# Kernel tuning notes

Hardware: AMD Instinct MI355X
Metric: run time of the kernel (lower is better)

The kernel has to match this reference:

```python
import jax, jax.numpy as jnp
import numpy as np

B, A, NB, BOND = 256, 100, 10, 110
AF, BF, H, DEPTH = 82, 6, 300, 3

def setup_inputs() -> dict:
    key = jax.random.key(0)
    ks = jax.random.split(key, 16)
    atom_feats = jax.random.normal(ks[0], (B, A, AF), dtype=jnp.float32)
    bond_feats = jax.random.normal(ks[1], (B, BOND, BF), dtype=jnp.float32)
    ag_b = jax.random.randint(ks[2], (B, A, NB, 1), 0, B, dtype=jnp.int32)
    ag_a = jax.random.randint(ks[3], (B, A, NB, 1), 0, A, dtype=jnp.int32)
    atom_graph = jnp.concatenate([ag_b, ag_a], axis=-1)
    bg_b = jax.random.randint(ks[4], (B, A, NB, 1), 0, B, dtype=jnp.int32)
    bg_e = jax.random.randint(ks[5], (B, A, NB, 1), 0, BOND, dtype=jnp.int32)
    bond_graph = jnp.concatenate([bg_b, bg_e], axis=-1)
    num_nbs = jax.random.randint(ks[6], (B, A), 0, NB + 1, dtype=jnp.int32)
    n_atoms = jax.random.randint(ks[7], (B,), 50, A + 1, dtype=jnp.int32)
    n_atoms = n_atoms.at[0].set(A)  # padding must equal n_atoms.max()
    sc = lambda i, o: (2.0 / (i + o)) ** 0.5
    w_fc1 = jax.random.normal(ks[8], (AF, H), dtype=jnp.float32) * sc(AF, H)
    w_nei = jax.random.normal(ks[9], (H + BF, H), dtype=jnp.float32) * sc(H + BF, H)
    b_nei = jnp.zeros((H,), dtype=jnp.float32)
    w_atom = jax.random.normal(ks[10], (2 * H, H), dtype=jnp.float32) * sc(2 * H, H)
    b_atom = jnp.zeros((H,), dtype=jnp.float32)
    w2a = jax.random.normal(ks[11], (H, H), dtype=jnp.float32) * sc(H, H)
    w2b = jax.random.normal(ks[12], (BF, H), dtype=jnp.float32) * sc(BF, H)
    w_fc2 = jax.random.normal(ks[13], (H, H), dtype=jnp.float32) * sc(H, H)
    return dict(atom_feats=atom_feats, bond_feats=bond_feats, w_fc1=w_fc1,
                w_nei=w_nei, b_nei=b_nei, w_atom=w_atom, b_atom=b_atom,
                w2a=w2a, w2b=w2b, w_fc2=w_fc2, atom_graph=atom_graph,
                bond_graph=bond_graph, num_nbs=num_nbs, n_atoms=n_atoms)

def reference(atom_feats, bond_feats, w_fc1, w_nei, b_nei, w_atom, b_atom,
              w2a, w2b, w_fc2, atom_graph, bond_graph, num_nbs, n_atoms):
    h = jax.nn.relu(atom_feats @ w_fc1)                      # [B,A,H]
    bondnei = bond_feats[bond_graph[..., 0], bond_graph[..., 1]]  # [B,A,NB,BF]
    mask_neis = (num_nbs[..., None] > jnp.arange(NB, dtype=jnp.int32))[..., None]
    mask_atoms = (n_atoms[:, None] > jnp.arange(A, dtype=jnp.int32))[..., None]
    for i in range(DEPTH):
        atomnei = h[atom_graph[..., 0], atom_graph[..., 1]]  # [B,A,NB,H]
        if i + 1 == DEPTH:
            nei = (atomnei @ w2a) * (bondnei @ w2b)          # [B,A,NB,H]
            nei = jnp.where(mask_neis, nei, 0.0).sum(-2)     # [B,A,H]
            local = (h @ w_fc2) * nei
            local = jnp.where(mask_atoms, local, 0.0)
        else:
            nei = jax.nn.relu(jnp.concatenate([atomnei, bondnei], -1) @ w_nei + b_nei)
            nei = jnp.where(mask_neis, nei, 0.0).sum(-2)
            h = jax.nn.relu(jnp.concatenate([h, nei], -1) @ w_atom + b_atom)
    return local
```

## Files before the change

### kernel.cpp

```cpp
#include <hip/hip_runtime.h>

#define B_    256
#define A_    100
#define NB_   10
#define BOND_ 110
#define AF_   82
#define BF_   6
#define H_    300
#define NP_   320
#define MA_   (B_ * A_)
#define MB_   (B_ * BOND_)
#define KP300 320
#define KP82  96

typedef __attribute__((ext_vector_type(8))) short short8;
typedef __attribute__((ext_vector_type(4))) float f32x4;

__device__ __forceinline__ ushort f2bf(float v) {
    union { float f; unsigned u; } x; x.f = v;
    unsigned r = x.u + 0x7fffu + ((x.u >> 16) & 1u);
    return (ushort)(r >> 16);
}
__device__ __forceinline__ float bf2f(ushort h) {
    union { float f; unsigned u; } x; x.u = ((unsigned)h) << 16;
    return x.f;
}

__device__ __forceinline__ void gload16(const void* g, void* l) {
    __builtin_amdgcn_global_load_lds(
        (const __attribute__((address_space(1))) void*)g,
        (__attribute__((address_space(3))) void*)l, 16, 0, 0);
}

template<bool DUAL, bool BIAS, bool RELU, int OUTMODE>
__global__ __launch_bounds__(256, 1) void mgemm_k(
    const ushort* __restrict__ aH, const ushort* __restrict__ aL,
    const ushort* __restrict__ fH, const ushort* __restrict__ fL,
    const ushort* __restrict__ aH2, const ushort* __restrict__ aL2,
    const ushort* __restrict__ fH2, const ushort* __restrict__ fL2,
    int KP,
    const float* __restrict__ bias,
    const float* __restrict__ E,
    const int*   __restrict__ n_atoms,
    ushort* __restrict__ oHi, ushort* __restrict__ oLo,
    float*  __restrict__ oF)
{
    __shared__ char lds[3 * 20480];
    const int tid  = threadIdx.x;
    const int lane = tid & 63;
    const int l16  = lane & 15;
    const int kg   = lane >> 4;
    const int w    = tid >> 6;
    const int rowbase = blockIdx.x * 100;

    const int nks   = KP >> 5;
    const int total = (DUAL ? 2 : 1) * nks;

    int st_row[5], st_choff[5], st_plane[5];
    #pragma unroll
    for (int q = 0; q < 5; ++q) {
        int g = q * 256 + tid;
        int plane = (g >= 640) ? 1 : 0;
        int local = g - plane * 640;
        int row = local / 5;
        int ch  = local % 5; if (ch == 4) ch = 3;
        int grow = rowbase + row; if (grow >= MA_) grow = MA_ - 1;
        st_row[q] = grow; st_choff[q] = ch * 16; st_plane[q] = plane;
    }

    auto stage = [&](int t) {
        int pass = (DUAL && t >= nks) ? 1 : 0;
        int ks   = t - (pass ? nks : 0);
        const ushort* SH = pass ? aH2 : aH;
        const ushort* SL = pass ? aL2 : aL;
        char* dst = (char*)lds + (t % 3) * 20480 + (tid & 192) * 16;
        #pragma unroll
        for (int q = 0; q < 5; ++q) {
            const ushort* src = (st_plane[q] ? SL : SH) + (size_t)st_row[q] * KP + ks * 32;
            gload16((const char*)src + st_choff[q], dst + q * 4096);
        }
    };

    f32x4 acc[7][5] = {};

    stage(0);
    for (int tk = 0; tk < total; ++tk) {
        short8 bh[5], bl[5];
        {
            int pass = (DUAL && tk >= nks) ? 1 : 0;
            int ks   = tk - (pass ? nks : 0);
            const ushort* FHp = pass ? fH2 : fH;
            const ushort* FLp = pass ? fL2 : fL;
            size_t base = ((size_t)ks * 20 + w * 5) * 512 + (size_t)lane * 8;
            #pragma unroll
            for (int c = 0; c < 5; ++c) {
                bh[c] = *(const short8*)(FHp + base + c * 512);
                bl[c] = *(const short8*)(FLp + base + c * 512);
            }
        }
        if (tk + 1 < total) stage(tk + 1);

        if (tk + 1 < total) { asm volatile("s_waitcnt vmcnt(5)" ::: "memory"); }
        else                { asm volatile("s_waitcnt vmcnt(0)" ::: "memory"); }
        __builtin_amdgcn_s_barrier();
        __builtin_amdgcn_sched_barrier(0);

        const char* ab = (const char*)lds + (tk % 3) * 20480;
        const int ao = l16 * 80 + kg * 16;
        #pragma unroll
        for (int rt = 0; rt < 7; ++rt) {
            short8 ah = *(const short8*)(ab + rt * 1280 + ao);
            short8 al = *(const short8*)(ab + 10240 + rt * 1280 + ao);
            #pragma unroll
            for (int c = 0; c < 5; ++c) {
                acc[rt][c] = __builtin_amdgcn_mfma_f32_16x16x32_bf16(ah, bh[c], acc[rt][c], 0, 0, 0);
                acc[rt][c] = __builtin_amdgcn_mfma_f32_16x16x32_bf16(al, bh[c], acc[rt][c], 0, 0, 0);
                acc[rt][c] = __builtin_amdgcn_mfma_f32_16x16x32_bf16(ah, bl[c], acc[rt][c], 0, 0, 0);
            }
        }
        __builtin_amdgcn_s_barrier();
    }

    float biasv[5];
    #pragma unroll
    for (int c = 0; c < 5; ++c) {
        int col = w * 80 + c * 16 + l16;
        biasv[c] = (BIAS && col < H_) ? bias[col] : 0.f;
    }
    #pragma unroll
    for (int rt = 0; rt < 7; ++rt) {
        #pragma unroll
        for (int c = 0; c < 5; ++c) {
            const int col = w * 80 + c * 16 + l16;
            #pragma unroll
            for (int r = 0; r < 4; ++r) {
                const int lrow = rt * 16 + kg * 4 + r;
                if (lrow >= 100) continue;
                const int row = rowbase + lrow;
                float v = acc[rt][c][r];
                if (BIAS) v += biasv[c];
                if (RELU) v = fmaxf(v, 0.f);
                if (OUTMODE == 0) {
                    ushort hi = f2bf(v);
                    ushort lo = f2bf(v - bf2f(hi));
                    size_t o = (size_t)row * NP_ + col;
                    oHi[o] = hi; oLo[o] = lo;
                } else if (OUTMODE == 1) {
                    oF[(size_t)row * NP_ + col] = v;
                } else {
                    if (col < H_) {
                        v *= E[(size_t)row * NP_ + col];
                        int b = row / A_;
                        int a = row - b * A_;
                        if (a >= n_atoms[b]) v = 0.f;
                        oF[(size_t)row * H_ + col] = v;
                    }
                }
            }
        }
    }
}

__global__ __launch_bounds__(256) void conv_wfrag_k(
    const float* __restrict__ src, int K, int KP,
    ushort* __restrict__ dH, ushort* __restrict__ dL)
{
    int idx = blockIdx.x * 256 + threadIdx.x;
    int nwords = (KP >> 5) * 20 * 64;
    if (idx >= nwords) return;
    int lane = idx & 63;
    int t  = idx >> 6;
    int ct = t % 20;
    int ks = t / 20;
    int col = ct * 16 + (lane & 15);
    int k0  = ks * 32 + (lane >> 4) * 8;
    short8 hv, lv;
    #pragma unroll
    for (int j = 0; j < 8; ++j) {
        int k = k0 + j;
        float v = (col < H_ && k < K) ? src[(size_t)k * H_ + col] : 0.f;
        ushort h = f2bf(v);
        hv[j] = (short)h;
        lv[j] = (short)f2bf(v - bf2f(h));
    }
    *(short8*)(dH + (size_t)idx * 8) = hv;
    *(short8*)(dL + (size_t)idx * 8) = lv;
}

__global__ __launch_bounds__(256) void conv_af_k(
    const float* __restrict__ src, ushort* __restrict__ dhi, ushort* __restrict__ dlo)
{
    int idx = blockIdx.x * 256 + threadIdx.x;
    if (idx >= MA_ * KP82) return;
    int row = idx / KP82, k = idx - row * KP82;
    float v = (k < AF_) ? src[(size_t)row * AF_ + k] : 0.f;
    ushort hi = f2bf(v);
    dhi[idx] = hi;
    dlo[idx] = f2bf(v - bf2f(hi));
}

__global__ __launch_bounds__(256) void bondmm_k(
    const float* __restrict__ bf, const float* __restrict__ wmat,
    const float* __restrict__ bias, float* __restrict__ out)
{
    int idx = blockIdx.x * 256 + threadIdx.x;
    if (idx >= MB_ * 80) return;
    int row = idx / 80, c4 = idx - row * 80;
    float4 s = make_float4(0.f, 0.f, 0.f, 0.f);
    if (c4 < 75) {
        int col = c4 * 4;
        if (bias) s = *(const float4*)(bias + col);
        #pragma unroll
        for (int k = 0; k < 6; ++k) {
            float b = bf[(size_t)row * 6 + k];
            float4 wv = *(const float4*)(wmat + (size_t)k * H_ + col);
            s.x = fmaf(b, wv.x, s.x); s.y = fmaf(b, wv.y, s.y);
            s.z = fmaf(b, wv.z, s.z); s.w = fmaf(b, wv.w, s.w);
        }
    }
    *(float4*)(out + (size_t)row * NP_ + c4 * 4) = s;
}

__global__ __launch_bounds__(256) void agg_relu_k(
    const float* __restrict__ hw, const float* __restrict__ bwn,
    const int* __restrict__ ag, const int* __restrict__ bg,
    const int* __restrict__ num_nbs,
    ushort* __restrict__ neiH, ushort* __restrict__ neiL)
{
    int idx = blockIdx.x * 256 + threadIdx.x;
    if (idx >= MA_ * 80) return;
    int ba = idx / 80, c4 = idx - ba * 80;
    int nn = num_nbs[ba];
    const int* agp = ag + (size_t)ba * NB_ * 2;
    const int* bgp = bg + (size_t)ba * NB_ * 2;
    float4 s = make_float4(0.f, 0.f, 0.f, 0.f);
    for (int n = 0; n < nn; ++n) {
        int arow = agp[2*n] * A_    + agp[2*n+1];
        int brow = bgp[2*n] * BOND_ + bgp[2*n+1];
        float4 hv = *(const float4*)(hw  + (size_t)arow * NP_ + c4 * 4);
        float4 bv = *(const float4*)(bwn + (size_t)brow * NP_ + c4 * 4);
        s.x += fmaxf(hv.x + bv.x, 0.f); s.y += fmaxf(hv.y + bv.y, 0.f);
        s.z += fmaxf(hv.z + bv.z, 0.f); s.w += fmaxf(hv.w + bv.w, 0.f);
    }
    size_t o = (size_t)ba * NP_ + c4 * 4;
    ushort4 hi, lo;
    hi.x = f2bf(s.x); lo.x = f2bf(s.x - bf2f(hi.x));
    hi.y = f2bf(s.y); lo.y = f2bf(s.y - bf2f(hi.y));
    hi.z = f2bf(s.z); lo.z = f2bf(s.z - bf2f(hi.z));
    hi.w = f2bf(s.w); lo.w = f2bf(s.w - bf2f(hi.w));
    *(ushort4*)(neiH + o) = hi;
    *(ushort4*)(neiL + o) = lo;
}

__global__ __launch_bounds__(256) void agg_prod_k(
    const float* __restrict__ hw2, const float* __restrict__ bw2,
    const int* __restrict__ ag, const int* __restrict__ bg,
    const int* __restrict__ num_nbs, float* __restrict__ neiF)
{
    int idx = blockIdx.x * 256 + threadIdx.x;
    if (idx >= MA_ * 80) return;
    int ba = idx / 80, c4 = idx - ba * 80;
    int nn = num_nbs[ba];
    const int* agp = ag + (size_t)ba * NB_ * 2;
    const int* bgp = bg + (size_t)ba * NB_ * 2;
    float4 s = make_float4(0.f, 0.f, 0.f, 0.f);
    for (int n = 0; n < nn; ++n) {
        int arow = agp[2*n] * A_    + agp[2*n+1];
        int brow = bgp[2*n] * BOND_ + bgp[2*n+1];
        float4 hv = *(const float4*)(hw2 + (size_t)arow * NP_ + c4 * 4);
        float4 bv = *(const float4*)(bw2 + (size_t)brow * NP_ + c4 * 4);
        s.x = fmaf(hv.x, bv.x, s.x); s.y = fmaf(hv.y, bv.y, s.y);
        s.z = fmaf(hv.z, bv.z, s.z); s.w = fmaf(hv.w, bv.w, s.w);
    }
    *(float4*)(neiF + (size_t)ba * NP_ + c4 * 4) = s;
}

extern "C" void kernel_launch(void* const* d_in, const int* in_sizes, int n_in,
                              void* d_out, int out_size, void* d_ws, size_t ws_size,
                              hipStream_t stream)
{
    const float* atom_feats = (const float*)d_in[0];
    const float* bond_feats = (const float*)d_in[1];
    const float* w_fc1      = (const float*)d_in[2];
    const float* w_nei      = (const float*)d_in[3];
    const float* b_nei      = (const float*)d_in[4];
    const float* w_atom     = (const float*)d_in[5];
    const float* b_atom     = (const float*)d_in[6];
    const float* w2a        = (const float*)d_in[7];
    const float* w2b        = (const float*)d_in[8];
    const float* w_fc2      = (const float*)d_in[9];
    const int*   atom_graph = (const int*)d_in[10];
    const int*   bond_graph = (const int*)d_in[11];
    const int*   num_nbs    = (const int*)d_in[12];
    const int*   n_atoms    = (const int*)d_in[13];
    float* out = (float*)d_out;
    (void)in_sizes; (void)n_in; (void)out_size; (void)ws_size;

    const size_t SZ_H16 = (size_t)MA_ * NP_ * 2;
    const size_t SZ_HF  = (size_t)MA_ * NP_ * 4;
    const size_t SZ_BWN = (size_t)MB_ * NP_ * 4;
    const size_t SZ_AF  = (size_t)MA_ * KP82 * 2;
    const size_t SZ_WT  = (size_t)NP_ * KP300 * 2;
    const size_t SZ_WT1 = (size_t)NP_ * KP82 * 2;
    char* p = (char*)d_ws;
    ushort* hA_h = (ushort*)p; p += SZ_H16;
    ushort* hA_l = (ushort*)p; p += SZ_H16;
    ushort* hB_h = (ushort*)p; p += SZ_H16;
    ushort* hB_l = (ushort*)p; p += SZ_H16;
    ushort* nei_h = (ushort*)p; p += SZ_H16;
    ushort* nei_l = (ushort*)p; p += SZ_H16;
    float* hwF = (float*)p; p += SZ_HF;
    float* bwn = (float*)p; p += SZ_BWN;
    ushort* af_h = (ushort*)p; p += SZ_AF;
    ushort* af_l = (ushort*)p; p += SZ_AF;
    ushort* wfc1_h = (ushort*)p; p += SZ_WT1;
    ushort* wfc1_l = (ushort*)p; p += SZ_WT1;
    ushort* wn1_h  = (ushort*)p; p += SZ_WT;
    ushort* wn1_l  = (ushort*)p; p += SZ_WT;
    ushort* wa1_h  = (ushort*)p; p += SZ_WT;
    ushort* wa1_l  = (ushort*)p; p += SZ_WT;
    ushort* wa2_h  = (ushort*)p; p += SZ_WT;
    ushort* wa2_l  = (ushort*)p; p += SZ_WT;
    ushort* w2a_h  = (ushort*)p; p += SZ_WT;
    ushort* w2a_l  = (ushort*)p; p += SZ_WT;
    ushort* wfc2_h = (ushort*)p; p += SZ_WT;
    ushort* wfc2_l = (ushort*)p; p += SZ_WT;
    float* neiF = (float*)hB_h;

    const dim3 blk(256);
    const dim3 gG(256);
    const int  aggG  = (MA_ * 80 + 255) / 256;
    const int  bondG = (MB_ * 80 + 255) / 256;
    const int  fw300 = ((KP300 >> 5) * 20 * 64 + 255) / 256;
    const int  fw96  = ((KP82  >> 5) * 20 * 64 + 255) / 256;

    conv_af_k<<<(MA_*KP82+255)/256, blk, 0, stream>>>(atom_feats, af_h, af_l);
    conv_wfrag_k<<<fw96,  blk, 0, stream>>>(w_fc1, AF_, KP82, wfc1_h, wfc1_l);
    conv_wfrag_k<<<fw300, blk, 0, stream>>>(w_nei,                 H_, KP300, wn1_h, wn1_l);
    conv_wfrag_k<<<fw300, blk, 0, stream>>>(w_atom,                H_, KP300, wa1_h, wa1_l);
    conv_wfrag_k<<<fw300, blk, 0, stream>>>(w_atom + (size_t)H_*H_, H_, KP300, wa2_h, wa2_l);
    conv_wfrag_k<<<fw300, blk, 0, stream>>>(w2a,                   H_, KP300, w2a_h, w2a_l);
    conv_wfrag_k<<<fw300, blk, 0, stream>>>(w_fc2,                 H_, KP300, wfc2_h, wfc2_l);

    bondmm_k<<<bondG, blk, 0, stream>>>(bond_feats, w_nei + (size_t)H_*H_, b_nei, bwn);

    mgemm_k<false,false,true,0><<<gG, blk, 0, stream>>>(
        af_h, af_l, wfc1_h, wfc1_l, nullptr,nullptr,nullptr,nullptr, KP82,
        nullptr, nullptr, nullptr, hA_h, hA_l, nullptr);

    ushort* hc_h = hA_h; ushort* hc_l = hA_l;
    ushort* hn_h = hB_h; ushort* hn_l = hB_l;
    for (int it = 0; it < 2; ++it) {
        mgemm_k<false,false,false,1><<<gG, blk, 0, stream>>>(
            hc_h, hc_l, wn1_h, wn1_l, nullptr,nullptr,nullptr,nullptr, KP300,
            nullptr, nullptr, nullptr, nullptr, nullptr, hwF);
        agg_relu_k<<<aggG, blk, 0, stream>>>(hwF, bwn, atom_graph, bond_graph, num_nbs, nei_h, nei_l);
        mgemm_k<true,true,true,0><<<gG, blk, 0, stream>>>(
            hc_h, hc_l, wa1_h, wa1_l, nei_h, nei_l, wa2_h, wa2_l, KP300,
            b_atom, nullptr, nullptr, hn_h, hn_l, nullptr);
        ushort* t;
        t = hc_h; hc_h = hn_h; hn_h = t;
        t = hc_l; hc_l = hn_l; hn_l = t;
    }

    bondmm_k<<<bondG, blk, 0, stream>>>(bond_feats, w2b, nullptr, bwn);
    mgemm_k<false,false,false,1><<<gG, blk, 0, stream>>>(
        hc_h, hc_l, w2a_h, w2a_l, nullptr,nullptr,nullptr,nullptr, KP300,
        nullptr, nullptr, nullptr, nullptr, nullptr, hwF);
    agg_prod_k<<<aggG, blk, 0, stream>>>(hwF, bwn, atom_graph, bond_graph, num_nbs, neiF);
    mgemm_k<false,false,false,2><<<gG, blk, 0, stream>>>(
        hc_h, hc_l, wfc2_h, wfc2_l, nullptr,nullptr,nullptr,nullptr, KP300,
        nullptr, neiF, n_atoms, nullptr, nullptr, out);
}
```

Measured before the change: 529.5 us.

## Shrink GEMM row tile to 64 rows for more blocks and occupancy

Changes the split-bf16 GEMM kernel from 100-row tiles (256 blocks) to 64-row tiles (400 blocks), with simpler staging (two 16-byte loads per thread) and a smaller LDS ring. Launch bounds allow two blocks per CU and the accumulator array shrinks from 7x5 to 4x5. The aim is better CU occupancy and load balance on a 256-CU part, at the cost of reloading the weight fragments more often. It also removes the trailing barrier in the k-loop, relying on the triple-buffered LDS ring to keep stage writes away from the buffer being read.

```diff
diff --git a/kernel.cpp b/kernel.cpp
--- a/kernel.cpp
+++ b/kernel.cpp
@@ -33,7 +33,7 @@
 }
 
 template<bool DUAL, bool BIAS, bool RELU, int OUTMODE>
-__global__ __launch_bounds__(256, 1) void mgemm_k(
+__global__ __launch_bounds__(256, 2) void mgemm_k(
     const ushort* __restrict__ aH, const ushort* __restrict__ aL,
     const ushort* __restrict__ fH, const ushort* __restrict__ fL,
     const ushort* __restrict__ aH2, const ushort* __restrict__ aL2,
@@ -45,43 +45,32 @@
     ushort* __restrict__ oHi, ushort* __restrict__ oLo,
     float*  __restrict__ oF)
 {
-    __shared__ char lds[3 * 20480];
+    __shared__ char lds[3 * 8192];
     const int tid  = threadIdx.x;
     const int lane = tid & 63;
     const int l16  = lane & 15;
     const int kg   = lane >> 4;
     const int w    = tid >> 6;
-    const int rowbase = blockIdx.x * 100;
+    const int rowbase = blockIdx.x * 64;
 
     const int nks   = KP >> 5;
     const int total = (DUAL ? 2 : 1) * nks;
 
-    int st_row[5], st_choff[5], st_plane[5];
-    #pragma unroll
-    for (int q = 0; q < 5; ++q) {
-        int g = q * 256 + tid;
-        int plane = (g >= 640) ? 1 : 0;
-        int local = g - plane * 640;
-        int row = local / 5;
-        int ch  = local % 5; if (ch == 4) ch = 3;
-        int grow = rowbase + row; if (grow >= MA_) grow = MA_ - 1;
-        st_row[q] = grow; st_choff[q] = ch * 16; st_plane[q] = plane;
-    }
+    const size_t srow = (size_t)(rowbase + (tid >> 2)) * KP;
+    const int    sch  = (tid & 3) * 8;
 
     auto stage = [&](int t) {
         int pass = (DUAL && t >= nks) ? 1 : 0;
         int ks   = t - (pass ? nks : 0);
         const ushort* SH = pass ? aH2 : aH;
         const ushort* SL = pass ? aL2 : aL;
-        char* dst = (char*)lds + (t % 3) * 20480 + (tid & 192) * 16;
-        #pragma unroll
-        for (int q = 0; q < 5; ++q) {
-            const ushort* src = (st_plane[q] ? SL : SH) + (size_t)st_row[q] * KP + ks * 32;
-            gload16((const char*)src + st_choff[q], dst + q * 4096);
-        }
+        char* dst = (char*)lds + (t % 3) * 8192 + (tid & 192) * 16;
+        gload16(SH + srow + ks * 32 + sch, dst);
+        gload16(SL + srow + ks * 32 + sch, dst + 4096);
     };
 
-    f32x4 acc[7][5] = {};
+    f32x4 acc[4][5] = {};
+    const int aoff = l16 * 64 + kg * 16;
 
     stage(0);
     for (int tk = 0; tk < total; ++tk) {
@@ -100,17 +89,16 @@
         }
         if (tk + 1 < total) stage(tk + 1);
 
-        if (tk + 1 < total) { asm volatile("s_waitcnt vmcnt(5)" ::: "memory"); }
+        if (tk + 1 < total) { asm volatile("s_waitcnt vmcnt(2)" ::: "memory"); }
         else                { asm volatile("s_waitcnt vmcnt(0)" ::: "memory"); }
         __builtin_amdgcn_s_barrier();
         __builtin_amdgcn_sched_barrier(0);
 
-        const char* ab = (const char*)lds + (tk % 3) * 20480;
-        const int ao = l16 * 80 + kg * 16;
+        const char* ab = (const char*)lds + (tk % 3) * 8192;
         #pragma unroll
-        for (int rt = 0; rt < 7; ++rt) {
-            short8 ah = *(const short8*)(ab + rt * 1280 + ao);
-            short8 al = *(const short8*)(ab + 10240 + rt * 1280 + ao);
+        for (int rt = 0; rt < 4; ++rt) {
+            short8 ah = *(const short8*)(ab +        rt * 1024 + aoff);
+            short8 al = *(const short8*)(ab + 4096 + rt * 1024 + aoff);
             #pragma unroll
             for (int c = 0; c < 5; ++c) {
                 acc[rt][c] = __builtin_amdgcn_mfma_f32_16x16x32_bf16(ah, bh[c], acc[rt][c], 0, 0, 0);
@@ -118,7 +106,6 @@
                 acc[rt][c] = __builtin_amdgcn_mfma_f32_16x16x32_bf16(ah, bl[c], acc[rt][c], 0, 0, 0);
             }
         }
-        __builtin_amdgcn_s_barrier();
     }
 
     float biasv[5];
@@ -128,15 +115,13 @@
         biasv[c] = (BIAS && col < H_) ? bias[col] : 0.f;
     }
     #pragma unroll
-    for (int rt = 0; rt < 7; ++rt) {
+    for (int rt = 0; rt < 4; ++rt) {
         #pragma unroll
         for (int c = 0; c < 5; ++c) {
             const int col = w * 80 + c * 16 + l16;
             #pragma unroll
             for (int r = 0; r < 4; ++r) {
-                const int lrow = rt * 16 + kg * 4 + r;
-                if (lrow >= 100) continue;
-                const int row = rowbase + lrow;
+                const int row = rowbase + rt * 16 + kg * 4 + r;
                 float v = acc[rt][c][r];
                 if (BIAS) v += biasv[c];
                 if (RELU) v = fmaxf(v, 0.f);
@@ -328,7 +313,7 @@
     float* neiF = (float*)hB_h;
 
     const dim3 blk(256);
-    const dim3 gG(256);
+    const dim3 gG(MA_ / 64);
     const int  aggG  = (MA_ * 80 + 255) / 256;
     const int  bondG = (MB_ * 80 + 255) / 256;
     const int  fw300 = ((KP300 >> 5) * 20 * 64 + 255) / 256;
```

New measurement: 454.5 us. 14.2% less time.
